# Kernel tuning notes

Hardware: AMD Instinct MI355X
Metric: run time of the kernel (lower is better)

## Reference

```python
import jax, jax.numpy as jnp
import numpy as np

HIDDEN = 256
N = 8192
TAU = 0.5


def setup_inputs() -> dict:
    key = jax.random.key(0)
    k1, k2, k3, k4, kw, kb = jax.random.split(key, 6)
    v1_embs = jax.random.normal(k1, (N, HIDDEN), dtype=jnp.float32)
    v2_embs = jax.random.normal(k2, (N, HIDDEN), dtype=jnp.float32)
    pos = jax.random.uniform(k3, (N, N), dtype=jnp.float32)
    neg = jax.random.uniform(k4, (N, N), dtype=jnp.float32)
    # xavier_normal_ with gain=1.414: std = gain * sqrt(2/(fan_in+fan_out))
    std = 1.414 * np.sqrt(2.0 / (HIDDEN + HIDDEN))
    W = jax.random.normal(kw, (HIDDEN, HIDDEN), dtype=jnp.float32) * std
    b = jnp.zeros((HIDDEN,), dtype=jnp.float32)
    return {"v1_embs": v1_embs, "v2_embs": v2_embs, "pos": pos, "neg": neg, "W": W, "b": b}


def _proj(x, W, b):
    # Linear + ELU
    return jax.nn.elu(x @ W.T + b)


def _sim(z1, z2, tau):
    # exp(cosine_similarity / tau) via outer product of norms
    n1 = jnp.linalg.norm(z1, axis=-1, keepdims=True)  # [N,1]
    n2 = jnp.linalg.norm(z2, axis=-1, keepdims=True)  # [N,1]
    num = z1 @ z2.T                                    # [N,N]
    den = n1 @ n2.T                                    # [N,N]
    return jnp.exp(num / den / tau)


def reference(v1_embs, v2_embs, pos, neg, W, b):
    z1 = _proj(v1_embs, W, b)
    z2 = _proj(v2_embs, W, b)
    m = _sim(z1, z2, TAU)              # [N,N]
    sim_pos = m * pos
    sim_neg = m * neg
    ratio = sim_pos.sum() / (sim_pos + sim_neg).sum()
    return -jnp.log(ratio)
```

## Files before the change

### kernel.cpp

```cpp
#include <hip/hip_runtime.h>
#include <hip/hip_bf16.h>

#define N 8192
#define H 256

typedef __attribute__((ext_vector_type(8))) short bf16x8;
typedef __attribute__((ext_vector_type(4))) float f32x4;
typedef __attribute__((ext_vector_type(4))) _Float16 h4;

__global__ __launch_bounds__(256) void convw_kernel(
    const float* __restrict__ W, __hip_bfloat16* __restrict__ Wb)
{
    int i = (blockIdx.x * 256 + threadIdx.x) * 4;
    float4 w = *(const float4*)(W + i);
    __hip_bfloat16 o[4] = {__float2bfloat16(w.x), __float2bfloat16(w.y),
                           __float2bfloat16(w.z), __float2bfloat16(w.w)};
    *(short4*)(Wb + i) = *(short4*)o;
}

__global__ __launch_bounds__(256) void proj_kernel(
    const float* __restrict__ v1, const float* __restrict__ v2,
    const __hip_bfloat16* __restrict__ Wb, const float* __restrict__ bias,
    __hip_bfloat16* __restrict__ zh1, __hip_bfloat16* __restrict__ zh2)
{
    const float* x = blockIdx.y ? v2 : v1;
    __hip_bfloat16* zh = blockIdx.y ? zh2 : zh1;
    int lane = threadIdx.x & 63, wave = threadIdx.x >> 6;
    int r16 = lane & 15, quad = lane >> 4;

    long arow = (long)blockIdx.x * 64 + wave * 16 + r16;
    const float* xr = x + arow * H + quad * 8;
    const __hip_bfloat16* wb = Wb + r16 * H + quad * 8;

    f32x4 acc[16] = {};
#pragma unroll
    for (int k8 = 0; k8 < 8; ++k8) {
        float4 xa = *(const float4*)(xr + k8 * 32);
        float4 xb = *(const float4*)(xr + k8 * 32 + 4);
        union { bf16x8 v; __hip_bfloat16 h[8]; } u;
        u.h[0] = __float2bfloat16(xa.x); u.h[1] = __float2bfloat16(xa.y);
        u.h[2] = __float2bfloat16(xa.z); u.h[3] = __float2bfloat16(xa.w);
        u.h[4] = __float2bfloat16(xb.x); u.h[5] = __float2bfloat16(xb.y);
        u.h[6] = __float2bfloat16(xb.z); u.h[7] = __float2bfloat16(xb.w);
#pragma unroll
        for (int nt = 0; nt < 16; ++nt) {
            bf16x8 bf = *(const bf16x8*)(wb + nt * 16 * H + k8 * 32);
            acc[nt] = __builtin_amdgcn_mfma_f32_16x16x32_bf16(u.v, bf, acc[nt], 0, 0, 0);
        }
    }

    float ss[4] = {};
#pragma unroll
    for (int nt = 0; nt < 16; ++nt) {
        float bc = bias[nt * 16 + r16];
#pragma unroll
        for (int g = 0; g < 4; ++g) {
            float v = acc[nt][g] + bc;
            v = v > 0.f ? v : (__expf(v) - 1.f);
            acc[nt][g] = v;
            ss[g] = fmaf(v, v, ss[g]);
        }
    }
    long crow0 = (long)blockIdx.x * 64 + wave * 16 + quad * 4;
#pragma unroll
    for (int g = 0; g < 4; ++g) {
        float s = ss[g];
#pragma unroll
        for (int o = 1; o < 16; o <<= 1) s += __shfl_xor(s, o);
        float inv = rsqrtf(s);
#pragma unroll
        for (int nt = 0; nt < 16; ++nt)
            zh[(crow0 + g) * H + nt * 16 + r16] = __float2bfloat16(acc[nt][g] * inv);
    }
}

__global__ __launch_bounds__(256) void contrast_kernel(
    const __hip_bfloat16* __restrict__ zh1, const __hip_bfloat16* __restrict__ zh2,
    const float* __restrict__ pos, const float* __restrict__ neg,
    float* __restrict__ bins)
{
    __shared__ _Float16 elds[128][132];
    int lane = threadIdx.x & 63;
    int wave = threadIdx.x >> 6;
    int wr = wave >> 1, wc = wave & 1;
    int r16 = lane & 15, quad = lane >> 4;
    long row0 = (long)blockIdx.x * 128 + wr * 64;
    long col0 = (long)blockIdx.y * 128 + wc * 64;

    f32x4 acc[4][4] = {};

    const __hip_bfloat16* ap = zh1 + (row0 + r16) * H + quad * 8;
    const __hip_bfloat16* bp = zh2 + (col0 + r16) * H + quad * 8;
#pragma unroll
    for (int k = 0; k < H; k += 32) {
        bf16x8 a[4], b[4];
#pragma unroll
        for (int t = 0; t < 4; ++t) a[t] = *(const bf16x8*)(ap + t * 16 * H + k);
#pragma unroll
        for (int t = 0; t < 4; ++t) b[t] = *(const bf16x8*)(bp + t * 16 * H + k);
#pragma unroll
        for (int mi = 0; mi < 4; ++mi)
#pragma unroll
            for (int nj = 0; nj < 4; ++nj)
                acc[mi][nj] = __builtin_amdgcn_mfma_f32_16x16x32_bf16(
                    a[mi], b[nj], acc[mi][nj], 0, 0, 0);
    }

#pragma unroll
    for (int mi = 0; mi < 4; ++mi) {
        int lrow = wr * 64 + mi * 16 + quad * 4;
#pragma unroll
        for (int nj = 0; nj < 4; ++nj) {
            int lcol = wc * 64 + nj * 16 + r16;
#pragma unroll
            for (int g = 0; g < 4; ++g)
                elds[lrow + g][lcol] = (_Float16)__expf(acc[mi][nj][g] * 2.0f);
        }
    }
    __syncthreads();

    const float* pb = pos + ((long)blockIdx.x * 128) * N + (long)blockIdx.y * 128;
    const float* nb = neg + ((long)blockIdx.x * 128) * N + (long)blockIdx.y * 128;
    float sp = 0.f, sn = 0.f;
#pragma unroll
    for (int half = 0; half < 2; ++half) {
        float4 pv[8], nv[8];
#pragma unroll
        for (int it = 0; it < 8; ++it) {
            int idx = threadIdx.x + (half * 8 + it) * 256;
            long r = idx >> 5;
            int c = (idx & 31) * 4;
            pv[it] = *(const float4*)(pb + r * N + c);
            nv[it] = *(const float4*)(nb + r * N + c);
        }
#pragma unroll
        for (int it = 0; it < 8; ++it) {
            int idx = threadIdx.x + (half * 8 + it) * 256;
            int r = idx >> 5;
            int c = (idx & 31) * 4;
            h4 e = *(const h4*)&elds[r][c];
            sp = fmaf((float)e.x, pv[it].x, sp);
            sp = fmaf((float)e.y, pv[it].y, sp);
            sp = fmaf((float)e.z, pv[it].z, sp);
            sp = fmaf((float)e.w, pv[it].w, sp);
            sn = fmaf((float)e.x, nv[it].x, sn);
            sn = fmaf((float)e.y, nv[it].y, sn);
            sn = fmaf((float)e.z, nv[it].z, sn);
            sn = fmaf((float)e.w, nv[it].w, sn);
        }
    }

#pragma unroll
    for (int o = 32; o > 0; o >>= 1) {
        sp += __shfl_down(sp, o);
        sn += __shfl_down(sn, o);
    }
    __shared__ float wsum[4][2];
    if (lane == 0) { wsum[wave][0] = sp; wsum[wave][1] = sn; }
    __syncthreads();
    if (threadIdx.x == 0) {
        float bsp = wsum[0][0] + wsum[1][0] + wsum[2][0] + wsum[3][0];
        float bsn = wsum[0][1] + wsum[1][1] + wsum[2][1] + wsum[3][1];
        int bin = blockIdx.x & 63;
        atomicAdd(&bins[bin], bsp);
        atomicAdd(&bins[64 + bin], bsn);
    }
}

__global__ void final_kernel(const float* __restrict__ bins, float* __restrict__ out)
{
    int lane = threadIdx.x;
    float sp = bins[lane], sn = bins[64 + lane];
#pragma unroll
    for (int o = 32; o > 0; o >>= 1) {
        sp += __shfl_down(sp, o);
        sn += __shfl_down(sn, o);
    }
    if (lane == 0) out[0] = -logf(sp / (sp + sn));
}

extern "C" void kernel_launch(void* const* d_in, const int* in_sizes, int n_in,
                              void* d_out, int out_size, void* d_ws, size_t ws_size,
                              hipStream_t stream)
{
    const float* v1   = (const float*)d_in[0];
    const float* v2   = (const float*)d_in[1];
    const float* pos  = (const float*)d_in[2];
    const float* neg  = (const float*)d_in[3];
    const float* W    = (const float*)d_in[4];
    const float* bias = (const float*)d_in[5];

    __hip_bfloat16* zh1 = (__hip_bfloat16*)d_ws;
    __hip_bfloat16* zh2 = zh1 + (size_t)N * H;
    char* p8 = (char*)d_ws + 2ull * N * H * sizeof(__hip_bfloat16);
    __hip_bfloat16* Wb = (__hip_bfloat16*)p8;
    float* bins = (float*)(p8 + (size_t)H * H * sizeof(__hip_bfloat16));

    hipMemsetAsync(bins, 0, 128 * sizeof(float), stream);
    convw_kernel<<<64, 256, 0, stream>>>(W, Wb);
    proj_kernel<<<dim3(N / 64, 2), 256, 0, stream>>>(v1, v2, Wb, bias, zh1, zh2);
    contrast_kernel<<<dim3(N / 128, N / 128), 256, 0, stream>>>(zh1, zh2, pos, neg, bins);
    final_kernel<<<1, 64, 0, stream>>>(bins, (float*)d_out);
}
```

Before: 639.3 us.

## Shrink contrast tiles to per-wave 64x32, issue pos/neg loads early, drop block syncs

Each block of the contrast kernel now covers a 128x64 tile, with each wave owning a private 64x32 sub-tile in its own LDS slice. The wave issues its pos/neg loads before writing exp values to LDS, so the fetch from HBM overlaps the exp work. Both __syncthreads are gone and each wave does its own atomicAdd. Launch bounds ask for 4 blocks per CU to raise occupancy on this memory-bound stream. The price is twice as many blocks, more redundant loads of zh1 (A-fragment reuse halves), and twice as many atomics.

```diff
diff --git a/kernel.cpp b/kernel.cpp
--- a/kernel.cpp
+++ b/kernel.cpp
@@ -74,80 +74,77 @@
     }
 }
 
-__global__ __launch_bounds__(256) void contrast_kernel(
+__global__ __launch_bounds__(256, 4) void contrast_kernel(
     const __hip_bfloat16* __restrict__ zh1, const __hip_bfloat16* __restrict__ zh2,
     const float* __restrict__ pos, const float* __restrict__ neg,
     float* __restrict__ bins)
 {
-    __shared__ _Float16 elds[128][132];
+    __shared__ _Float16 elds[4][64][36];
     int lane = threadIdx.x & 63;
     int wave = threadIdx.x >> 6;
     int wr = wave >> 1, wc = wave & 1;
     int r16 = lane & 15, quad = lane >> 4;
     long row0 = (long)blockIdx.x * 128 + wr * 64;
-    long col0 = (long)blockIdx.y * 128 + wc * 64;
+    long col0 = (long)blockIdx.y * 64 + wc * 32;
 
-    f32x4 acc[4][4] = {};
+    f32x4 acc[4][2] = {};
 
     const __hip_bfloat16* ap = zh1 + (row0 + r16) * H + quad * 8;
     const __hip_bfloat16* bp = zh2 + (col0 + r16) * H + quad * 8;
 #pragma unroll
     for (int k = 0; k < H; k += 32) {
-        bf16x8 a[4], b[4];
+        bf16x8 a[4], b[2];
 #pragma unroll
-        for (int t = 0; t < 4; ++t) a[t] = *(const bf16x8*)(ap + t * 16 * H + k);
+        for (int mi = 0; mi < 4; ++mi) a[mi] = *(const bf16x8*)(ap + mi * 16 * H + k);
 #pragma unroll
-        for (int t = 0; t < 4; ++t) b[t] = *(const bf16x8*)(bp + t * 16 * H + k);
+        for (int nj = 0; nj < 2; ++nj) b[nj] = *(const bf16x8*)(bp + nj * 16 * H + k);
 #pragma unroll
         for (int mi = 0; mi < 4; ++mi)
 #pragma unroll
-            for (int nj = 0; nj < 4; ++nj)
+            for (int nj = 0; nj < 2; ++nj)
                 acc[mi][nj] = __builtin_amdgcn_mfma_f32_16x16x32_bf16(
                     a[mi], b[nj], acc[mi][nj], 0, 0, 0);
     }
 
+    const float* pb = pos + row0 * N + col0;
+    const float* nb = neg + row0 * N + col0;
+    float4 pv[8], nv[8];
+#pragma unroll
+    for (int it = 0; it < 8; ++it) {
+        int idx = lane + it * 64;
+        long r = idx >> 3;
+        int c = (idx & 7) * 4;
+        pv[it] = *(const float4*)(pb + r * N + c);
+        nv[it] = *(const float4*)(nb + r * N + c);
+    }
+
 #pragma unroll
     for (int mi = 0; mi < 4; ++mi) {
-        int lrow = wr * 64 + mi * 16 + quad * 4;
 #pragma unroll
-        for (int nj = 0; nj < 4; ++nj) {
-            int lcol = wc * 64 + nj * 16 + r16;
+        for (int nj = 0; nj < 2; ++nj) {
+            int lcol = nj * 16 + r16;
 #pragma unroll
             for (int g = 0; g < 4; ++g)
-                elds[lrow + g][lcol] = (_Float16)__expf(acc[mi][nj][g] * 2.0f);
+                elds[wave][mi * 16 + quad * 4 + g][lcol] =
+                    (_Float16)__expf(acc[mi][nj][g] * 2.0f);
         }
     }
-    __syncthreads();
 
-    const float* pb = pos + ((long)blockIdx.x * 128) * N + (long)blockIdx.y * 128;
-    const float* nb = neg + ((long)blockIdx.x * 128) * N + (long)blockIdx.y * 128;
     float sp = 0.f, sn = 0.f;
 #pragma unroll
-    for (int half = 0; half < 2; ++half) {
-        float4 pv[8], nv[8];
-#pragma unroll
-        for (int it = 0; it < 8; ++it) {
-            int idx = threadIdx.x + (half * 8 + it) * 256;
-            long r = idx >> 5;
-            int c = (idx & 31) * 4;
-            pv[it] = *(const float4*)(pb + r * N + c);
-            nv[it] = *(const float4*)(nb + r * N + c);
-        }
-#pragma unroll
-        for (int it = 0; it < 8; ++it) {
-            int idx = threadIdx.x + (half * 8 + it) * 256;
-            int r = idx >> 5;
-            int c = (idx & 31) * 4;
-            h4 e = *(const h4*)&elds[r][c];
-            sp = fmaf((float)e.x, pv[it].x, sp);
-            sp = fmaf((float)e.y, pv[it].y, sp);
-            sp = fmaf((float)e.z, pv[it].z, sp);
-            sp = fmaf((float)e.w, pv[it].w, sp);
-            sn = fmaf((float)e.x, nv[it].x, sn);
-            sn = fmaf((float)e.y, nv[it].y, sn);
-            sn = fmaf((float)e.z, nv[it].z, sn);
-            sn = fmaf((float)e.w, nv[it].w, sn);
-        }
+    for (int it = 0; it < 8; ++it) {
+        int idx = lane + it * 64;
+        int r = idx >> 3;
+        int c = (idx & 7) * 4;
+        h4 e = *(const h4*)&elds[wave][r][c];
+        sp = fmaf((float)e.x, pv[it].x, sp);
+        sp = fmaf((float)e.y, pv[it].y, sp);
+        sp = fmaf((float)e.z, pv[it].z, sp);
+        sp = fmaf((float)e.w, pv[it].w, sp);
+        sn = fmaf((float)e.x, nv[it].x, sn);
+        sn = fmaf((float)e.y, nv[it].y, sn);
+        sn = fmaf((float)e.z, nv[it].z, sn);
+        sn = fmaf((float)e.w, nv[it].w, sn);
     }
 
 #pragma unroll
@@ -155,15 +152,10 @@
         sp += __shfl_down(sp, o);
         sn += __shfl_down(sn, o);
     }
-    __shared__ float wsum[4][2];
-    if (lane == 0) { wsum[wave][0] = sp; wsum[wave][1] = sn; }
-    __syncthreads();
-    if (threadIdx.x == 0) {
-        float bsp = wsum[0][0] + wsum[1][0] + wsum[2][0] + wsum[3][0];
-        float bsn = wsum[0][1] + wsum[1][1] + wsum[2][1] + wsum[3][1];
+    if (lane == 0) {
         int bin = blockIdx.x & 63;
-        atomicAdd(&bins[bin], bsp);
-        atomicAdd(&bins[64 + bin], bsn);
+        atomicAdd(&bins[bin], sp);
+        atomicAdd(&bins[64 + bin], sn);
     }
 }
 
@@ -199,6 +191,6 @@
     hipMemsetAsync(bins, 0, 128 * sizeof(float), stream);
     convw_kernel<<<64, 256, 0, stream>>>(W, Wb);
     proj_kernel<<<dim3(N / 64, 2), 256, 0, stream>>>(v1, v2, Wb, bias, zh1, zh2);
-    contrast_kernel<<<dim3(N / 128, N / 128), 256, 0, stream>>>(zh1, zh2, pos, neg, bins);
+    contrast_kernel<<<dim3(N / 128, N / 64), 256, 0, stream>>>(zh1, zh2, pos, neg, bins);
     final_kernel<<<1, 64, 0, stream>>>(bins, (float*)d_out);
 }
```

Result: slower. 660.7 us (+3.3%).

## Split contrast into exp-matrix materialization and streaming reduce; repartition projection

Applied to the files above, without the earlier changes.

When the workspace is large enough, the fused contrast kernel is split in two. One kernel computes the exp-similarity tile and writes it as a full fp16 N×N matrix. A separate streaming kernel then reads that matrix along with pos and neg in fully contiguous order and reduces them. The projection kernel now spreads each 16-row block across four waves by output columns and combines the row norms through shared memory, which gives four times as many blocks. The split adds a 128MB write and read of the intermediate matrix in exchange for cleaner memory streaming, and the active path depends on the workspace size.

```diff
diff --git a/kernel.cpp b/kernel.cpp
--- a/kernel.cpp
+++ b/kernel.cpp
@@ -23,16 +23,17 @@
     const __hip_bfloat16* __restrict__ Wb, const float* __restrict__ bias,
     __hip_bfloat16* __restrict__ zh1, __hip_bfloat16* __restrict__ zh2)
 {
+    __shared__ float partial[4][16];
     const float* x = blockIdx.y ? v2 : v1;
     __hip_bfloat16* zh = blockIdx.y ? zh2 : zh1;
-    int lane = threadIdx.x & 63, wave = threadIdx.x >> 6;
+    int lane = threadIdx.x & 63, wc = threadIdx.x >> 6;
     int r16 = lane & 15, quad = lane >> 4;
 
-    long arow = (long)blockIdx.x * 64 + wave * 16 + r16;
-    const float* xr = x + arow * H + quad * 8;
-    const __hip_bfloat16* wb = Wb + r16 * H + quad * 8;
-
-    f32x4 acc[16] = {};
+    long row0 = (long)blockIdx.x * 16;
+    const float* xr = x + (row0 + r16) * H + quad * 8;
+    const __hip_bfloat16* wb = Wb + (wc * 64 + r16) * H + quad * 8;
+
+    f32x4 acc[4] = {};
 #pragma unroll
     for (int k8 = 0; k8 < 8; ++k8) {
         float4 xa = *(const float4*)(xr + k8 * 32);
@@ -43,41 +44,49 @@
         u.h[4] = __float2bfloat16(xb.x); u.h[5] = __float2bfloat16(xb.y);
         u.h[6] = __float2bfloat16(xb.z); u.h[7] = __float2bfloat16(xb.w);
 #pragma unroll
-        for (int nt = 0; nt < 16; ++nt) {
-            bf16x8 bf = *(const bf16x8*)(wb + nt * 16 * H + k8 * 32);
-            acc[nt] = __builtin_amdgcn_mfma_f32_16x16x32_bf16(u.v, bf, acc[nt], 0, 0, 0);
+        for (int j = 0; j < 4; ++j) {
+            bf16x8 bf = *(const bf16x8*)(wb + j * 16 * H + k8 * 32);
+            acc[j] = __builtin_amdgcn_mfma_f32_16x16x32_bf16(u.v, bf, acc[j], 0, 0, 0);
         }
     }
 
     float ss[4] = {};
 #pragma unroll
-    for (int nt = 0; nt < 16; ++nt) {
-        float bc = bias[nt * 16 + r16];
+    for (int j = 0; j < 4; ++j) {
+        float bc = bias[wc * 64 + j * 16 + r16];
 #pragma unroll
         for (int g = 0; g < 4; ++g) {
-            float v = acc[nt][g] + bc;
+            float v = acc[j][g] + bc;
             v = v > 0.f ? v : (__expf(v) - 1.f);
-            acc[nt][g] = v;
+            acc[j][g] = v;
             ss[g] = fmaf(v, v, ss[g]);
         }
     }
-    long crow0 = (long)blockIdx.x * 64 + wave * 16 + quad * 4;
 #pragma unroll
     for (int g = 0; g < 4; ++g) {
-        float s = ss[g];
-#pragma unroll
-        for (int o = 1; o < 16; o <<= 1) s += __shfl_xor(s, o);
-        float inv = rsqrtf(s);
-#pragma unroll
-        for (int nt = 0; nt < 16; ++nt)
-            zh[(crow0 + g) * H + nt * 16 + r16] = __float2bfloat16(acc[nt][g] * inv);
-    }
-}
-
-__global__ __launch_bounds__(256) void contrast_kernel(
+#pragma unroll
+        for (int o = 1; o < 16; o <<= 1) ss[g] += __shfl_xor(ss[g], o);
+    }
+    if (r16 == 0) {
+#pragma unroll
+        for (int g = 0; g < 4; ++g) partial[wc][quad * 4 + g] = ss[g];
+    }
+    __syncthreads();
+#pragma unroll
+    for (int g = 0; g < 4; ++g) {
+        int row = quad * 4 + g;
+        float tot = partial[0][row] + partial[1][row] + partial[2][row] + partial[3][row];
+        float inv = rsqrtf(tot);
+#pragma unroll
+        for (int j = 0; j < 4; ++j)
+            zh[(row0 + row) * H + wc * 64 + j * 16 + r16] =
+                __float2bfloat16(acc[j][g] * inv);
+    }
+}
+
+__global__ __launch_bounds__(256) void ecomp_kernel(
     const __hip_bfloat16* __restrict__ zh1, const __hip_bfloat16* __restrict__ zh2,
-    const float* __restrict__ pos, const float* __restrict__ neg,
-    float* __restrict__ bins)
+    _Float16* __restrict__ e)
 {
     __shared__ _Float16 elds[128][132];
     int lane = threadIdx.x & 63;
@@ -88,7 +97,6 @@
     long col0 = (long)blockIdx.y * 128 + wc * 64;
 
     f32x4 acc[4][4] = {};
-
     const __hip_bfloat16* ap = zh1 + (row0 + r16) * H + quad * 8;
     const __hip_bfloat16* bp = zh2 + (col0 + r16) * H + quad * 8;
 #pragma unroll
@@ -106,6 +114,104 @@
                     a[mi], b[nj], acc[mi][nj], 0, 0, 0);
     }
 
+#pragma unroll
+    for (int mi = 0; mi < 4; ++mi) {
+        int lrow = wr * 64 + mi * 16 + quad * 4;
+#pragma unroll
+        for (int nj = 0; nj < 4; ++nj) {
+            int lcol = wc * 64 + nj * 16 + r16;
+#pragma unroll
+            for (int g = 0; g < 4; ++g)
+                elds[lrow + g][lcol] = (_Float16)__expf(acc[mi][nj][g] * 2.0f);
+        }
+    }
+    __syncthreads();
+
+    _Float16* eb = e + ((long)blockIdx.x * 128) * N + (long)blockIdx.y * 128;
+#pragma unroll
+    for (int it = 0; it < 16; ++it) {
+        int idx = threadIdx.x + it * 256;
+        long r = idx >> 5;
+        int c = (idx & 31) * 4;
+        *(h4*)(eb + r * N + c) = *(const h4*)&elds[r][c];
+    }
+}
+
+__global__ __launch_bounds__(256) void reduce_kernel(
+    const _Float16* __restrict__ e, const float* __restrict__ pos,
+    const float* __restrict__ neg, float* __restrict__ bins)
+{
+    size_t t = (size_t)blockIdx.x * 256 + threadIdx.x;
+    float sp = 0.f, sn = 0.f;
+    for (int k = 0; k < 32; k += 4) {
+        h4 ev[4]; float4 pv[4], nv[4];
+#pragma unroll
+        for (int j = 0; j < 4; ++j) {
+            size_t base = (t + (size_t)(k + j) * 524288) * 4;
+            ev[j] = *(const h4*)(e + base);
+            pv[j] = *(const float4*)(pos + base);
+            nv[j] = *(const float4*)(neg + base);
+        }
+#pragma unroll
+        for (int j = 0; j < 4; ++j) {
+            sp = fmaf((float)ev[j].x, pv[j].x, sp);
+            sp = fmaf((float)ev[j].y, pv[j].y, sp);
+            sp = fmaf((float)ev[j].z, pv[j].z, sp);
+            sp = fmaf((float)ev[j].w, pv[j].w, sp);
+            sn = fmaf((float)ev[j].x, nv[j].x, sn);
+            sn = fmaf((float)ev[j].y, nv[j].y, sn);
+            sn = fmaf((float)ev[j].z, nv[j].z, sn);
+            sn = fmaf((float)ev[j].w, nv[j].w, sn);
+        }
+    }
+#pragma unroll
+    for (int o = 32; o > 0; o >>= 1) {
+        sp += __shfl_down(sp, o);
+        sn += __shfl_down(sn, o);
+    }
+    __shared__ float wsum[4][2];
+    int lane = threadIdx.x & 63, wave = threadIdx.x >> 6;
+    if (lane == 0) { wsum[wave][0] = sp; wsum[wave][1] = sn; }
+    __syncthreads();
+    if (threadIdx.x == 0) {
+        float bsp = wsum[0][0] + wsum[1][0] + wsum[2][0] + wsum[3][0];
+        float bsn = wsum[0][1] + wsum[1][1] + wsum[2][1] + wsum[3][1];
+        int bin = blockIdx.x & 63;
+        atomicAdd(&bins[bin], bsp);
+        atomicAdd(&bins[64 + bin], bsn);
+    }
+}
+
+__global__ __launch_bounds__(256) void contrast_kernel(
+    const __hip_bfloat16* __restrict__ zh1, const __hip_bfloat16* __restrict__ zh2,
+    const float* __restrict__ pos, const float* __restrict__ neg,
+    float* __restrict__ bins)
+{
+    __shared__ _Float16 elds[128][132];
+    int lane = threadIdx.x & 63;
+    int wave = threadIdx.x >> 6;
+    int wr = wave >> 1, wc = wave & 1;
+    int r16 = lane & 15, quad = lane >> 4;
+    long row0 = (long)blockIdx.x * 128 + wr * 64;
+    long col0 = (long)blockIdx.y * 128 + wc * 64;
+
+    f32x4 acc[4][4] = {};
+    const __hip_bfloat16* ap = zh1 + (row0 + r16) * H + quad * 8;
+    const __hip_bfloat16* bp = zh2 + (col0 + r16) * H + quad * 8;
+#pragma unroll
+    for (int k = 0; k < H; k += 32) {
+        bf16x8 a[4], b[4];
+#pragma unroll
+        for (int t = 0; t < 4; ++t) a[t] = *(const bf16x8*)(ap + t * 16 * H + k);
+#pragma unroll
+        for (int t = 0; t < 4; ++t) b[t] = *(const bf16x8*)(bp + t * 16 * H + k);
+#pragma unroll
+        for (int mi = 0; mi < 4; ++mi)
+#pragma unroll
+            for (int nj = 0; nj < 4; ++nj)
+                acc[mi][nj] = __builtin_amdgcn_mfma_f32_16x16x32_bf16(
+                    a[mi], b[nj], acc[mi][nj], 0, 0, 0);
+    }
 #pragma unroll
     for (int mi = 0; mi < 4; ++mi) {
         int lrow = wr * 64 + mi * 16 + quad * 4;
@@ -138,18 +244,17 @@
             int idx = threadIdx.x + (half * 8 + it) * 256;
             int r = idx >> 5;
             int c = (idx & 31) * 4;
-            h4 e = *(const h4*)&elds[r][c];
-            sp = fmaf((float)e.x, pv[it].x, sp);
-            sp = fmaf((float)e.y, pv[it].y, sp);
-            sp = fmaf((float)e.z, pv[it].z, sp);
-            sp = fmaf((float)e.w, pv[it].w, sp);
-            sn = fmaf((float)e.x, nv[it].x, sn);
-            sn = fmaf((float)e.y, nv[it].y, sn);
-            sn = fmaf((float)e.z, nv[it].z, sn);
-            sn = fmaf((float)e.w, nv[it].w, sn);
-        }
-    }
-
+            h4 ev = *(const h4*)&elds[r][c];
+            sp = fmaf((float)ev.x, pv[it].x, sp);
+            sp = fmaf((float)ev.y, pv[it].y, sp);
+            sp = fmaf((float)ev.z, pv[it].z, sp);
+            sp = fmaf((float)ev.w, pv[it].w, sp);
+            sn = fmaf((float)ev.x, nv[it].x, sn);
+            sn = fmaf((float)ev.y, nv[it].y, sn);
+            sn = fmaf((float)ev.z, nv[it].z, sn);
+            sn = fmaf((float)ev.w, nv[it].w, sn);
+        }
+    }
 #pragma unroll
     for (int o = 32; o > 0; o >>= 1) {
         sp += __shfl_down(sp, o);
@@ -190,15 +295,27 @@
     const float* W    = (const float*)d_in[4];
     const float* bias = (const float*)d_in[5];
 
-    __hip_bfloat16* zh1 = (__hip_bfloat16*)d_ws;
-    __hip_bfloat16* zh2 = zh1 + (size_t)N * H;
-    char* p8 = (char*)d_ws + 2ull * N * H * sizeof(__hip_bfloat16);
-    __hip_bfloat16* Wb = (__hip_bfloat16*)p8;
-    float* bins = (float*)(p8 + (size_t)H * H * sizeof(__hip_bfloat16));
+    const size_t ebytes = (size_t)N * N * sizeof(_Float16);
+    const size_t zbytes = (size_t)N * H * sizeof(__hip_bfloat16);
+    const size_t need_big = ebytes + 2 * zbytes + (size_t)H * H * 2 + 512;
+    bool big = ws_size >= need_big;
+
+    char* p = (char*)d_ws;
+    _Float16* e = nullptr;
+    if (big) { e = (_Float16*)p; p += ebytes; }
+    __hip_bfloat16* zh1 = (__hip_bfloat16*)p;           p += zbytes;
+    __hip_bfloat16* zh2 = (__hip_bfloat16*)p;           p += zbytes;
+    __hip_bfloat16* Wb  = (__hip_bfloat16*)p;           p += (size_t)H * H * 2;
+    float* bins = (float*)p;
 
     hipMemsetAsync(bins, 0, 128 * sizeof(float), stream);
     convw_kernel<<<64, 256, 0, stream>>>(W, Wb);
-    proj_kernel<<<dim3(N / 64, 2), 256, 0, stream>>>(v1, v2, Wb, bias, zh1, zh2);
-    contrast_kernel<<<dim3(N / 128, N / 128), 256, 0, stream>>>(zh1, zh2, pos, neg, bins);
+    proj_kernel<<<dim3(N / 16, 2), 256, 0, stream>>>(v1, v2, Wb, bias, zh1, zh2);
+    if (big) {
+        ecomp_kernel<<<dim3(N / 128, N / 128), 256, 0, stream>>>(zh1, zh2, e);
+        reduce_kernel<<<2048, 256, 0, stream>>>(e, pos, neg, bins);
+    } else {
+        contrast_kernel<<<dim3(N / 128, N / 128), 256, 0, stream>>>(zh1, zh2, pos, neg, bins);
+    }
     final_kernel<<<1, 64, 0, stream>>>(bins, (float*)d_out);
 }
```

Result: slower. 713.6 us (+11.6%).
